# Kernel tuning notes

Measured on AMD Instinct MI355X. Metric: run time of the kernel, lower is better.

Reference implementation:

```python
import jax, jax.numpy as jnp
import numpy as np

N_NODES = 50000
NEG_SLOPE = 0.2

def _leaky(x):
    return jnp.where(x > 0, x, NEG_SLOPE * x)

def _magic_conv(h, src, dst, edge_attr, anet_W, anet_b, mlp_W, mlp_b, eps):
    # align edge features to node dim: [E, d_in]
    e = edge_attr @ anet_W + anet_b
    # message: relu(x_j + edge), gather from source nodes
    msg = jax.nn.relu(h[src] + e)
    # scatter-add aggregate to target nodes: [N, d_in]
    agg = jax.ops.segment_sum(msg, dst, num_segments=N_NODES)
    # GIN-style update: cat([agg, (1+eps)*x]) -> Linear -> LeakyReLU(0.2)
    z = jnp.concatenate([agg, (1.0 + eps) * h], axis=-1) @ mlp_W + mlp_b
    return _leaky(z)

def setup_inputs() -> dict:
    key = jax.random.key(0)
    ks = jax.random.split(key, 16)
    E, D, DE = 800000, 128, 64
    inp = {
        "x": jax.random.normal(ks[0], (N_NODES, D), dtype=jnp.float32),
        "edge_index": jax.random.randint(ks[1], (2, E), 0, N_NODES, dtype=jnp.int64),
        "edge_attr": jax.random.normal(ks[2], (E, DE), dtype=jnp.float32),
    }
    s = lambda d: 1.0 / np.sqrt(d)
    # conv layer 0 (128 -> 128) and layer 1 (128 -> 128)
    for l, k0 in [(0, 3), (1, 8)]:
        inp[f"anet_W{l}"] = jax.random.uniform(ks[k0], (DE, D), jnp.float32, -s(DE), s(DE))
        inp[f"anet_b{l}"] = jax.random.uniform(ks[k0 + 1], (D,), jnp.float32, -s(DE), s(DE))
        inp[f"mlp_W{l}"] = jax.random.uniform(ks[k0 + 2], (2 * D, D), jnp.float32, -s(2 * D), s(2 * D))
        inp[f"mlp_b{l}"] = jax.random.uniform(ks[k0 + 3], (D,), jnp.float32, -s(2 * D), s(2 * D))
        inp[f"eps{l}"] = jnp.full((1,), 1e-4, dtype=jnp.float32)
    # link predictor: Linear(128->128) + LeakyReLU, Linear(128->2)
    inp["lp_W1"] = jax.random.uniform(ks[13], (D, D), jnp.float32, -s(D), s(D))
    inp["lp_b1"] = jax.random.uniform(ks[14], (D,), jnp.float32, -s(D), s(D))
    inp["lp_W2"] = jax.random.uniform(ks[15], (D, 2), jnp.float32, -s(D), s(D))
    inp["lp_b2"] = jnp.zeros((2,), dtype=jnp.float32)
    return inp

def reference(x, edge_index, edge_attr, anet_W0, anet_b0, mlp_W0, mlp_b0, eps0,
              anet_W1, anet_b1, mlp_W1, mlp_b1, eps1,
              lp_W1, lp_b1, lp_W2, lp_b2):
    src = edge_index[0]
    dst = edge_index[1]
    h = _magic_conv(x, src, dst, edge_attr, anet_W0, anet_b0, mlp_W0, mlp_b0, eps0)
    h = _magic_conv(h, src, dst, edge_attr, anet_W1, anet_b1, mlp_W1, mlp_b1, eps1)
    h = jax.nn.relu(h)
    # MULT embed reduction over edge endpoints: [E, 128]
    h_edge = h[src] * h[dst]
    z = _leaky(h_edge @ lp_W1 + lp_b1)
    logits = z @ lp_W2 + lp_b2
    yhat = jax.nn.softmax(logits, axis=-1)
    return (h_edge, yhat)
```

## Files before the change

kernel.cpp:

```cpp
#include <hip/hip_runtime.h>
#include <math.h>

#define NNODES 50000
#define DIM 128
#define DEDGE 64

typedef __attribute__((ext_vector_type(8))) short bf16x8;
typedef __attribute__((ext_vector_type(4))) float f32x4;
typedef __attribute__((ext_vector_type(2))) float f32x2;

__device__ __forceinline__ float bf_lo(unsigned u) { return __builtin_bit_cast(float, u << 16); }
__device__ __forceinline__ float bf_hi(unsigned u) { return __builtin_bit_cast(float, u & 0xFFFF0000u); }
__device__ __forceinline__ float bf_s(short s) {
    return __builtin_bit_cast(float, ((unsigned)(unsigned short)s) << 16);
}
__device__ __forceinline__ unsigned short f2b_rtn(float f) {
    unsigned u = __builtin_bit_cast(unsigned, f);
    u += 0x7FFFu + ((u >> 16) & 1u);
    return (unsigned short)(u >> 16);
}

__global__ void detect_mode_kernel(const void* __restrict__ ei, int* __restrict__ flag) {
    __shared__ int bad;
    if (threadIdx.x == 0) bad = 0;
    __syncthreads();
    const long long* p = (const long long*)ei;
    int localbad = 0;
    for (int i = threadIdx.x; i < 4096; i += blockDim.x) {
        long long v = p[i];
        if (v < 0 || v >= NNODES) localbad = 1;
    }
    if (localbad) atomicOr(&bad, 1);
    __syncthreads();
    if (threadIdx.x == 0) *flag = bad ? 0 : 1;
}

__device__ __forceinline__ int load_idx(const void* ei, long long pos, int mode64) {
    if (mode64) return (int)((const long long*)ei)[pos];
    return ((const int*)ei)[pos];
}

__global__ void prep_weights(const float* __restrict__ aW0, const float* __restrict__ aW1,
                             const float* __restrict__ mW0, const float* __restrict__ mW1,
                             const float* __restrict__ lpW1,
                             const float* __restrict__ eps0p, const float* __restrict__ eps1p,
                             short* __restrict__ wt)
{
    int i = blockIdx.x * 256 + threadIdx.x;
    const float* src; int K, off, f;
    float scale_hi = 1.0f;
    if (i < 8192)        { src = aW0;  K = 64;  off = 0;     f = i; }
    else if (i < 16384)  { src = aW1;  K = 64;  off = 8192;  f = i - 8192; }
    else if (i < 49152)  { src = mW0;  K = 256; off = 16384; f = i - 16384;
                           scale_hi = 1.0f + eps0p[0]; }
    else if (i < 81920)  { src = mW1;  K = 256; off = 49152; f = i - 49152;
                           scale_hi = 1.0f + eps1p[0]; }
    else                 { src = lpW1; K = 128; off = 81920; f = i - 81920; }
    const int NKC = K >> 5;
    int j = f & 7, l = (f >> 3) & 63, c = f >> 9;
    int kc = c % NKC, n = c / NKC;
    int col = n * 16 + (l & 15);
    int k = kc * 32 + ((l >> 4) << 3) + j;
    float v = src[k * DIM + col];
    if (k >= 128) v *= scale_hi;
    wt[off + f] = (short)f2b_rtn(v);
}

__global__ void f32_to_bf16_kernel(const float* __restrict__ in,
                                   unsigned short* __restrict__ out, long long n)
{
    long long i = ((long long)blockIdx.x * 256 + threadIdx.x) * 8;
    if (i >= n) return;
    f32x4 a = *(const f32x4*)(in + i);
    f32x4 b = *(const f32x4*)(in + i + 4);
    unsigned short v[8];
#pragma unroll
    for (int t = 0; t < 4; t++) { v[t] = f2b_rtn(a[t]); v[4 + t] = f2b_rtn(b[t]); }
    unsigned p0 = v[0] | ((unsigned)v[1] << 16);
    unsigned p1 = v[2] | ((unsigned)v[3] << 16);
    unsigned p2 = v[4] | ((unsigned)v[5] << 16);
    unsigned p3 = v[6] | ((unsigned)v[7] << 16);
    f32x4 pk = {__builtin_bit_cast(float, p0), __builtin_bit_cast(float, p1),
                __builtin_bit_cast(float, p2), __builtin_bit_cast(float, p3)};
    *(f32x4*)(out + i) = pk;
}

__global__ void hist_kernel(const void* __restrict__ ei, const int* __restrict__ modep,
                            int* __restrict__ counts, int E)
{
    const int mode64 = *modep;
    for (int e = blockIdx.x * 256 + threadIdx.x; e < E; e += gridDim.x * 256)
        atomicAdd(&counts[load_idx(ei, (long long)E + e, mode64)], 1);
}

__global__ __launch_bounds__(1024) void scan1_kernel(const int* __restrict__ counts,
                                                     int* __restrict__ cursor,
                                                     int* __restrict__ bsums)
{
    __shared__ int part[1024];
    const int t = threadIdx.x;
    const int i = blockIdx.x * 1024 + t;
    int v = (i < NNODES) ? counts[i] : 0;
    part[t] = v;
    __syncthreads();
    for (int d = 1; d < 1024; d <<= 1) {
        int u = (t >= d) ? part[t - d] : 0;
        __syncthreads();
        part[t] += u;
        __syncthreads();
    }
    if (i < NNODES) cursor[i] = part[t] - v;
    if (t == 1023) bsums[blockIdx.x] = part[1023];
}

__global__ void scan2_kernel(int* __restrict__ bsums, int nb)
{
    if (threadIdx.x == 0 && blockIdx.x == 0) {
        int run = 0;
        for (int b = 0; b < nb; b++) { int c = bsums[b]; bsums[b] = run; run += c; }
    }
}

__global__ __launch_bounds__(1024) void scan3_kernel(int* __restrict__ cursor,
                                                     const int* __restrict__ bsums)
{
    const int i = blockIdx.x * 1024 + threadIdx.x;
    if (i < NNODES) cursor[i] += bsums[blockIdx.x];
}

__global__ void scatter_kernel(const void* __restrict__ ei, const int* __restrict__ modep,
                               int* __restrict__ cursor, int* __restrict__ perm,
                               int* __restrict__ srcs, int* __restrict__ dsts, int E)
{
    const int mode64 = *modep;
    for (int e = blockIdx.x * 256 + threadIdx.x; e < E; e += gridDim.x * 256) {
        int d = load_idx(ei, (long long)E + e, mode64);
        int s = load_idx(ei, e, mode64);
        int pos = atomicAdd(&cursor[d], 1);
        perm[pos] = e;
        srcs[pos] = s;
        dsts[pos] = d;
    }
}

__global__ void eattr_sort_bf16(const float* __restrict__ eattr, const int* __restrict__ perm,
                                unsigned short* __restrict__ out, int E)
{
    long long i = ((long long)blockIdx.x * 256 + threadIdx.x) * 8;
    if (i >= (long long)E * DEDGE) return;
    long long pos = i >> 6;
    int k = (int)(i & 63);
    long long eid = perm[pos];
    f32x4 a = *(const f32x4*)(eattr + eid * DEDGE + k);
    f32x4 b = *(const f32x4*)(eattr + eid * DEDGE + k + 4);
    unsigned short v[8];
#pragma unroll
    for (int t = 0; t < 4; t++) { v[t] = f2b_rtn(a[t]); v[4 + t] = f2b_rtn(b[t]); }
    unsigned p0 = v[0] | ((unsigned)v[1] << 16);
    unsigned p1 = v[2] | ((unsigned)v[3] << 16);
    unsigned p2 = v[4] | ((unsigned)v[5] << 16);
    unsigned p3 = v[6] | ((unsigned)v[7] << 16);
    f32x4 pk = {__builtin_bit_cast(float, p0), __builtin_bit_cast(float, p1),
                __builtin_bit_cast(float, p2), __builtin_bit_cast(float, p3)};
    __builtin_nontemporal_store(pk, (f32x4*)(out + i));
}

__global__ __launch_bounds__(256, 4) void edge_msg_sorted(
    const unsigned short* __restrict__ hb, const unsigned short* __restrict__ eattrs,
    const int* __restrict__ srcs, const int* __restrict__ dsts,
    const short* __restrict__ Wb,
    const float* __restrict__ bvec, float* __restrict__ agg, int E)
{
    __shared__ float e_lds[4][16][132];
    const int lane = threadIdx.x & 63;
    const int w = threadIdx.x >> 6;
    const int lg = lane >> 4, lr = lane & 15;
    const long long p0 = ((long long)blockIdx.x * 4 + w) * 32;
    if (p0 >= E) return;

    float bias[8];
#pragma unroll
    for (int n = 0; n < 8; n++) bias[n] = bvec[n * 16 + lr];

    float a0 = 0.f, a1 = 0.f;
    int prev = -1;
    const bool fullwave = (p0 + 32 <= E);

#pragma unroll
    for (int st = 0; st < 2; st++) {
        const long long t0 = p0 + st * 16;
        if (t0 >= E) break;
        const long long pos = (t0 + lr < E) ? (t0 + lr) : (E - 1);
        const int sidx = srcs[pos];
        const int didx = dsts[pos];

        f32x4 acc[8];
#pragma unroll
        for (int n = 0; n < 8; n++) {
            float b = bias[n];
            acc[n] = (f32x4){b, b, b, b};
        }
        bf16x8 a[2];
#pragma unroll
        for (int kc = 0; kc < 2; kc++)
            a[kc] = __builtin_nontemporal_load(
                (const bf16x8*)(eattrs + pos * DEDGE + kc * 32 + lg * 8));

#pragma unroll
        for (int n = 0; n < 8; n++) {
#pragma unroll
            for (int kc = 0; kc < 2; kc++) {
                bf16x8 bh = *(const bf16x8*)(Wb + ((n * 2 + kc) * 64 + lane) * 8);
                acc[n] = __builtin_amdgcn_mfma_f32_16x16x32_bf16(a[kc], bh, acc[n], 0, 0, 0);
            }
        }
#pragma unroll
        for (int n = 0; n < 8; n++)
#pragma unroll
            for (int r = 0; r < 4; r++)
                e_lds[w][lg * 4 + r][n * 16 + lr] = acc[n][r];

        if (fullwave) {
            unsigned gu[16];
            int dvs[16];
#pragma unroll
            for (int r = 0; r < 16; r++) {
                int si = __shfl(sidx, r);
                gu[r] = *(const unsigned*)&hb[(long long)si * DIM + 2 * lane];
            }
#pragma unroll
            for (int r = 0; r < 16; r++) dvs[r] = __shfl(didx, r);
#pragma unroll
            for (int r = 0; r < 16; r++) {
                f32x2 ev = *(const f32x2*)&e_lds[w][r][2 * lane];
                float m0 = fmaxf(ev.x + bf_lo(gu[r]), 0.f);
                float m1 = fmaxf(ev.y + bf_hi(gu[r]), 0.f);
                if (dvs[r] != prev && prev >= 0) {
                    float* d = &agg[(long long)prev * DIM + 2 * lane];
                    unsafeAtomicAdd(d, a0);
                    unsafeAtomicAdd(d + 1, a1);
                    a0 = 0.f; a1 = 0.f;
                }
                a0 += m0; a1 += m1; prev = dvs[r];
            }
        } else {
            for (int r = 0; r < 16; r++) {
                if (t0 + r >= E) break;
                int di = __shfl(didx, r);
                int si = __shfl(sidx, r);
                f32x2 ev = *(const f32x2*)&e_lds[w][r][2 * lane];
                unsigned u = *(const unsigned*)&hb[(long long)si * DIM + 2 * lane];
                float m0 = fmaxf(ev.x + bf_lo(u), 0.f);
                float m1 = fmaxf(ev.y + bf_hi(u), 0.f);
                if (di != prev && prev >= 0) {
                    float* d = &agg[(long long)prev * DIM + 2 * lane];
                    unsafeAtomicAdd(d, a0);
                    unsafeAtomicAdd(d + 1, a1);
                    a0 = 0.f; a1 = 0.f;
                }
                a0 += m0; a1 += m1; prev = di;
            }
        }
    }
    if (prev >= 0) {
        float* d = &agg[(long long)prev * DIM + 2 * lane];
        unsafeAtomicAdd(d, a0);
        unsafeAtomicAdd(d + 1, a1);
    }
}

__global__ __launch_bounds__(256, 4) void node_update_mfma(
    const float* __restrict__ agg, const unsigned short* __restrict__ hb,
    const short* __restrict__ Wb, const float* __restrict__ bvec,
    unsigned short* __restrict__ houtb, int relu_flag)
{
    __shared__ float st[4][16][132];
    const int lane = threadIdx.x & 63;
    const int w = threadIdx.x >> 6;
    const int lg = lane >> 4, lr = lane & 15;
    const int n0 = (blockIdx.x * 4 + w) * 16;
    if (n0 >= NNODES) return;
    const int arow = (n0 + lr < NNODES) ? (n0 + lr) : (NNODES - 1);

    f32x4 acc[8];
#pragma unroll
    for (int n = 0; n < 8; n++) {
        float b = bvec[n * 16 + lr];
        acc[n] = (f32x4){b, b, b, b};
    }
#pragma unroll
    for (int kc = 0; kc < 8; kc++) {
        bf16x8 av;
        if (kc < 4) {
            const int k = kc * 32 + lg * 8;
            f32x4 v0 = __builtin_nontemporal_load((const f32x4*)(agg + (long long)arow * DIM + k));
            f32x4 v1 = __builtin_nontemporal_load((const f32x4*)(agg + (long long)arow * DIM + k + 4));
#pragma unroll
            for (int i = 0; i < 4; i++) {
                av[i] = (short)f2b_rtn(v0[i]);
                av[4 + i] = (short)f2b_rtn(v1[i]);
            }
        } else {
            av = *(const bf16x8*)(hb + (long long)arow * DIM + (kc - 4) * 32 + lg * 8);
        }
#pragma unroll
        for (int n = 0; n < 8; n++) {
            bf16x8 bh = *(const bf16x8*)(Wb + ((n * 8 + kc) * 64 + lane) * 8);
            acc[n] = __builtin_amdgcn_mfma_f32_16x16x32_bf16(av, bh, acc[n], 0, 0, 0);
        }
    }
#pragma unroll
    for (int n = 0; n < 8; n++) {
#pragma unroll
        for (int r = 0; r < 4; r++) {
            float z = acc[n][r];
            z = relu_flag ? fmaxf(z, 0.f) : (z > 0.f ? z : 0.2f * z);
            st[w][lg * 4 + r][n * 16 + lr] = z;
        }
    }
    for (int r = 0; r < 16; r++) {
        int row = n0 + r;
        if (row >= NNODES) break;
        f32x2 v = *(const f32x2*)&st[w][r][2 * lane];
        unsigned pk = (unsigned)f2b_rtn(v.x) | ((unsigned)f2b_rtn(v.y) << 16);
        *(unsigned*)&houtb[(long long)row * DIM + 2 * lane] = pk;
    }
}

__global__ __launch_bounds__(256, 6) void edge_head_mfma(
    const unsigned short* __restrict__ hb, const void* __restrict__ ei,
    const int* __restrict__ modep,
    const short* __restrict__ W1b, const float* __restrict__ b1,
    const float* __restrict__ W2, const float* __restrict__ b2,
    float* __restrict__ out_he, float* __restrict__ out_y, int E)
{
    const int mode64 = *modep;
    const int lane = threadIdx.x & 63;
    const int w = threadIdx.x >> 6;
    const int lg = lane >> 4, lr = lane & 15;
    const long long e0 = ((long long)blockIdx.x * 4 + w) * 16;
    if (e0 >= E) return;
    const bool full = (e0 + 16 <= E);
    const long long erow = (full || e0 + lr < E) ? (e0 + lr) : (E - 1);
    int si = load_idx(ei, erow, mode64);
    int di = load_idx(ei, (long long)E + erow, mode64);

    f32x4 acc[8];
#pragma unroll
    for (int n = 0; n < 8; n++) {
        float b = b1[n * 16 + lr];
        acc[n] = (f32x4){b, b, b, b};
    }
    bf16x8 ab[4];
#pragma unroll
    for (int kc = 0; kc < 4; kc++) {
        const int k = kc * 32 + lg * 8;
        bf16x8 hs = *(const bf16x8*)(hb + (long long)si * DIM + k);
        bf16x8 hd = *(const bf16x8*)(hb + (long long)di * DIM + k);
        f32x4 p0, p1;
#pragma unroll
        for (int i = 0; i < 4; i++) {
            p0[i] = bf_s(hs[i]) * bf_s(hd[i]);
            p1[i] = bf_s(hs[4 + i]) * bf_s(hd[4 + i]);
        }
        if (full || e0 + lr < E) {
            __builtin_nontemporal_store(p0, (f32x4*)(out_he + erow * DIM + k));
            __builtin_nontemporal_store(p1, (f32x4*)(out_he + erow * DIM + k + 4));
        }
#pragma unroll
        for (int i = 0; i < 4; i++) {
            ab[kc][i] = (short)f2b_rtn(p0[i]);
            ab[kc][4 + i] = (short)f2b_rtn(p1[i]);
        }
    }
#pragma unroll
    for (int n = 0; n < 8; n++) {
#pragma unroll
        for (int kc = 0; kc < 4; kc++) {
            bf16x8 bh = *(const bf16x8*)(W1b + ((n * 4 + kc) * 64 + lane) * 8);
            acc[n] = __builtin_amdgcn_mfma_f32_16x16x32_bf16(ab[kc], bh, acc[n], 0, 0, 0);
        }
    }
    float q0[4] = {0.f, 0.f, 0.f, 0.f}, q1[4] = {0.f, 0.f, 0.f, 0.f};
#pragma unroll
    for (int n = 0; n < 8; n++) {
        float w2a = W2[(n * 16 + lr) * 2 + 0];
        float w2b = W2[(n * 16 + lr) * 2 + 1];
#pragma unroll
        for (int r = 0; r < 4; r++) {
            float z = acc[n][r];
            z = z > 0.f ? z : 0.2f * z;
            q0[r] = fmaf(z, w2a, q0[r]);
            q1[r] = fmaf(z, w2b, q1[r]);
        }
    }
#pragma unroll
    for (int m = 1; m < 16; m <<= 1) {
#pragma unroll
        for (int r = 0; r < 4; r++) {
            q0[r] += __shfl_xor(q0[r], m);
            q1[r] += __shfl_xor(q1[r], m);
        }
    }
    float c0 = b2[0], c1 = b2[1];
    float s0[4], s1[4];
#pragma unroll
    for (int r = 0; r < 4; r++) {
        float l0 = q0[r] + c0, l1 = q1[r] + c1;
        float mx = fmaxf(l0, l1);
        float x0 = expf(l0 - mx), x1 = expf(l1 - mx);
        float inv = 1.f / (x0 + x1);
        s0[r] = x0 * inv;
        s1[r] = x1 * inv;
    }
    if (full) {
        float ea = (lane & 2) ? s0[1] : s0[0];
        float eb = (lane & 2) ? s0[3] : s0[2];
        float ec = (lane & 2) ? s1[1] : s1[0];
        float ed = (lane & 2) ? s1[3] : s1[2];
        float e0v = (lane & 4) ? eb : ea;
        float e1v = (lane & 4) ? ed : ec;
        float ex = (lane & 1) ? e1v : e0v;
        float v = __shfl(ex, ((lane >> 3) << 4) + (lane & 7));
        if (lane < 32)
            __builtin_nontemporal_store(v, &out_y[e0 * 2 + lane]);
    } else if (lr == 0) {
#pragma unroll
        for (int r = 0; r < 4; r++) {
            long long e = e0 + lg * 4 + r;
            if (e < E) {
                out_y[e * 2 + 0] = s0[r];
                out_y[e * 2 + 1] = s1[r];
            }
        }
    }
}

extern "C" void kernel_launch(void* const* d_in, const int* in_sizes, int n_in,
                              void* d_out, int out_size, void* d_ws, size_t ws_size,
                              hipStream_t stream)
{
    const float* x     = (const float*)d_in[0];
    const void*  ei    = d_in[1];
    const float* eattr = (const float*)d_in[2];
    const float* aW0   = (const float*)d_in[3];
    const float* ab0   = (const float*)d_in[4];
    const float* mW0   = (const float*)d_in[5];
    const float* mb0   = (const float*)d_in[6];
    const float* eps0  = (const float*)d_in[7];
    const float* aW1   = (const float*)d_in[8];
    const float* ab1   = (const float*)d_in[9];
    const float* mW1   = (const float*)d_in[10];
    const float* mb1   = (const float*)d_in[11];
    const float* eps1  = (const float*)d_in[12];
    const float* lpW1  = (const float*)d_in[13];
    const float* lpb1  = (const float*)d_in[14];
    const float* lpW2  = (const float*)d_in[15];
    const float* lpb2  = (const float*)d_in[16];

    const int E = in_sizes[1] / 2;
    const long long NTAB = (long long)NNODES * DIM;

    float* wsf  = (float*)d_ws;
    int*   flag = (int*)d_ws;
    float* agg  = wsf + 64;
    short* wt   = (short*)(agg + NTAB);
    unsigned short* xb_h2b = (unsigned short*)(wt + 98304);
    unsigned short* h1b    = xb_h2b + NTAB;
    int* counts = (int*)(h1b + NTAB);
    int* cursor = counts + 50048;
    int* bsums  = cursor + 50048;
    int* perm   = bsums + 64;
    int* srcs   = perm + E;
    int* dsts   = srcs + E;
    unsigned short* eattrs = (unsigned short*)(dsts + E);

    float* out_he = (float*)d_out;
    float* out_y  = out_he + (long long)E * DIM;

    const short* aW0b  = wt;
    const short* aW1b  = wt + 8192;
    const short* mW0b  = wt + 16384;
    const short* mW1b  = wt + 49152;
    const short* lpW1b = wt + 81920;

    detect_mode_kernel<<<1, 256, 0, stream>>>(ei, flag);
    prep_weights<<<384, 256, 0, stream>>>(aW0, aW1, mW0, mW1, lpW1, eps0, eps1, wt);
    f32_to_bf16_kernel<<<(int)(NTAB / 8 / 256), 256, 0, stream>>>(x, xb_h2b, NTAB);

    hipMemsetAsync(counts, 0, 50048 * sizeof(int), stream);
    hist_kernel<<<1024, 256, 0, stream>>>(ei, flag, counts, E);
    const int sblocks = (NNODES + 1023) / 1024;
    scan1_kernel<<<sblocks, 1024, 0, stream>>>(counts, cursor, bsums);
    scan2_kernel<<<1, 64, 0, stream>>>(bsums, sblocks);
    scan3_kernel<<<sblocks, 1024, 0, stream>>>(cursor, bsums);
    scatter_kernel<<<1024, 256, 0, stream>>>(ei, flag, cursor, perm, srcs, dsts, E);
    eattr_sort_bf16<<<(E * DEDGE / 8 + 255) / 256, 256, 0, stream>>>(eattr, perm, eattrs, E);

    const int eblocks32 = (E + 127) / 128;
    const int eblocks16 = (E + 63) / 64;
    const int nblocks = (NNODES + 63) / 64;

    hipMemsetAsync(agg, 0, NTAB * sizeof(float), stream);
    edge_msg_sorted<<<eblocks32, 256, 0, stream>>>(xb_h2b, eattrs, srcs, dsts,
                                                   aW0b, ab0, agg, E);
    node_update_mfma<<<nblocks, 256, 0, stream>>>(agg, xb_h2b, mW0b, mb0, h1b, 0);

    hipMemsetAsync(agg, 0, NTAB * sizeof(float), stream);
    edge_msg_sorted<<<eblocks32, 256, 0, stream>>>(h1b, eattrs, srcs, dsts,
                                                   aW1b, ab1, agg, E);
    node_update_mfma<<<nblocks, 256, 0, stream>>>(agg, h1b, mW1b, mb1, xb_h2b, 1);

    edge_head_mfma<<<eblocks16, 256, 0, stream>>>(xb_h2b, ei, flag, lpW1b, lpb1, lpW2, lpb2,
                                                  out_he, out_y, E);
}
```

Measured before the change: 568.6 us.

## Split h_edge output write into separate coalesced kernel before edge head

```diff
diff --git a/kernel.cpp b/kernel.cpp
--- a/kernel.cpp
+++ b/kernel.cpp
@@ -327,12 +327,41 @@
     }
 }
 
+__global__ __launch_bounds__(256) void he_write_kernel(
+    const unsigned short* __restrict__ hb, const void* __restrict__ ei,
+    const int* __restrict__ modep, float* __restrict__ out_he, int E)
+{
+    const int mode64 = *modep;
+    const int lane = threadIdx.x & 63;
+    const int w = threadIdx.x >> 6;
+    const int half = lane >> 5;
+    const int col4 = (lane & 31) * 4;
+    const long long nw = (long long)gridDim.x * 4;
+
+    for (long long e0 = ((long long)blockIdx.x * 4 + w) * 8; e0 < E; e0 += nw * 8) {
+#pragma unroll
+        for (int t = 0; t < 4; t++) {
+            long long e = e0 + 2 * t + half;
+            if (e >= E) break;
+            int si = load_idx(ei, e, mode64);
+            int di = load_idx(ei, (long long)E + e, mode64);
+            unsigned s0 = *(const unsigned*)&hb[(long long)si * DIM + col4];
+            unsigned s1 = *(const unsigned*)&hb[(long long)si * DIM + col4 + 2];
+            unsigned d0 = *(const unsigned*)&hb[(long long)di * DIM + col4];
+            unsigned d1 = *(const unsigned*)&hb[(long long)di * DIM + col4 + 2];
+            f32x4 p = { bf_lo(s0) * bf_lo(d0), bf_hi(s0) * bf_hi(d0),
+                        bf_lo(s1) * bf_lo(d1), bf_hi(s1) * bf_hi(d1) };
+            __builtin_nontemporal_store(p, (f32x4*)(out_he + e * DIM + col4));
+        }
+    }
+}
+
 __global__ __launch_bounds__(256, 6) void edge_head_mfma(
     const unsigned short* __restrict__ hb, const void* __restrict__ ei,
     const int* __restrict__ modep,
     const short* __restrict__ W1b, const float* __restrict__ b1,
     const float* __restrict__ W2, const float* __restrict__ b2,
-    float* __restrict__ out_he, float* __restrict__ out_y, int E)
+    float* __restrict__ out_y, int E)
 {
     const int mode64 = *modep;
     const int lane = threadIdx.x & 63;
@@ -357,21 +386,9 @@
         const int k = kc * 32 + lg * 8;
         bf16x8 hs = *(const bf16x8*)(hb + (long long)si * DIM + k);
         bf16x8 hd = *(const bf16x8*)(hb + (long long)di * DIM + k);
-        f32x4 p0, p1;
-#pragma unroll
-        for (int i = 0; i < 4; i++) {
-            p0[i] = bf_s(hs[i]) * bf_s(hd[i]);
-            p1[i] = bf_s(hs[4 + i]) * bf_s(hd[4 + i]);
-        }
-        if (full || e0 + lr < E) {
-            __builtin_nontemporal_store(p0, (f32x4*)(out_he + erow * DIM + k));
-            __builtin_nontemporal_store(p1, (f32x4*)(out_he + erow * DIM + k + 4));
-        }
-#pragma unroll
-        for (int i = 0; i < 4; i++) {
-            ab[kc][i] = (short)f2b_rtn(p0[i]);
-            ab[kc][4 + i] = (short)f2b_rtn(p1[i]);
-        }
+#pragma unroll
+        for (int i = 0; i < 8; i++)
+            ab[kc][i] = (short)f2b_rtn(bf_s(hs[i]) * bf_s(hd[i]));
     }
 #pragma unroll
     for (int n = 0; n < 8; n++) {
@@ -511,6 +528,7 @@
                                                    aW1b, ab1, agg, E);
     node_update_mfma<<<nblocks, 256, 0, stream>>>(agg, h1b, mW1b, mb1, xb_h2b, 1);
 
+    he_write_kernel<<<4096, 256, 0, stream>>>(xb_h2b, ei, flag, out_he, E);
     edge_head_mfma<<<eblocks16, 256, 0, stream>>>(xb_h2b, ei, flag, lpW1b, lpb1, lpW2, lpb2,
-                                                  out_he, out_y, E);
-}
+                                                  out_y, E);
+}
```

Result: slower. 630.1 us (+10.8%).
